# Kernel tuning notes

Measured on AMD Instinct MI355X. Metric: run time of the kernel, lower is better.

## Reference

```python
import jax, jax.numpy as jnp
import numpy as np

N = 100000
E = 1600000
C_IN = 128
C_HID = 128


def setup_inputs() -> dict:
    key = jax.random.key(0)
    ks = jax.random.split(key, 6)
    x = jax.random.normal(ks[0], (N, C_IN), dtype=jnp.float32)
    edge_index = jax.random.randint(ks[1], (2, E), 0, N, dtype=jnp.int64)
    # GCNConv params: linear weight + bias per layer (glorot-ish scale)
    W1 = jax.random.normal(ks[2], (C_IN, C_HID), dtype=jnp.float32) / np.sqrt(C_IN)
    b1 = jnp.zeros((C_HID,), dtype=jnp.float32)
    W2 = jax.random.normal(ks[3], (C_HID, C_HID), dtype=jnp.float32) / np.sqrt(C_HID)
    b2 = jnp.zeros((C_HID,), dtype=jnp.float32)
    return {"x": x, "edge_index": edge_index, "W1": W1, "b1": b1, "W2": W2, "b2": b2}


def _gcn_conv(x, W, b, src, dst, n_nodes):
    # PyG GCNConv: h = D^{-1/2} (A + I) D^{-1/2} (x W) + b
    h = x @ W  # [N, C_out]
    # add self-loops
    loop = jnp.arange(n_nodes, dtype=src.dtype)
    s = jnp.concatenate([src, loop])
    d = jnp.concatenate([dst, loop])
    ones = jnp.ones(s.shape[0], dtype=h.dtype)
    deg = jax.ops.segment_sum(ones, d, num_segments=n_nodes)  # in-degree incl self-loop
    dinv = jnp.where(deg > 0, jax.lax.rsqrt(deg), 0.0)
    norm = dinv[s] * dinv[d]  # [E+N]
    msg = h[s] * norm[:, None]  # gather + scale
    out = jax.ops.segment_sum(msg, d, num_segments=n_nodes)  # scatter-add
    return out + b


def reference(x, edge_index, W1, b1, W2, b2):
    src, dst = edge_index[0], edge_index[1]
    h = jax.nn.relu(_gcn_conv(x, W1, b1, src, dst, N))
    h = jax.nn.relu(_gcn_conv(h, W2, b2, src, dst, N))
    return h
```

## Files before the change

kernel.cpp:

```cpp
#include <hip/hip_runtime.h>
#include <hip/hip_bf16.h>

#define GCN_N 100000
#define GB1 1563
#define NBUCK 782
#define BCAP 4096
#define KPWG 391

typedef unsigned short u16;
typedef unsigned int u32;
typedef float f32x4 __attribute__((ext_vector_type(4)));
typedef short bf16x8 __attribute__((ext_vector_type(8)));

union v16 { uint4 u; bf16x8 h; };

__device__ inline u16 f2bf(float f) {
    u32 u = __float_as_uint(f);
    return (u16)((u + 0x7fffu + ((u >> 16) & 1u)) >> 16);
}
__device__ inline u32 pack2(float a, float b) {
    return (u32)f2bf(a) | ((u32)f2bf(b) << 16);
}
__device__ inline float bf_lo(u32 u) { return __uint_as_float(u << 16); }
__device__ inline float bf_hi(u32 u) { return __uint_as_float(u & 0xffff0000u); }

__device__ inline void addu8(float* a, float4 v) {
    u32 u;
    u = __float_as_uint(v.x); a[0] += bf_lo(u); a[1] += bf_hi(u);
    u = __float_as_uint(v.y); a[2] += bf_lo(u); a[3] += bf_hi(u);
    u = __float_as_uint(v.z); a[4] += bf_lo(u); a[5] += bf_hi(u);
    u = __float_as_uint(v.w); a[6] += bf_lo(u); a[7] += bf_hi(u);
}
__device__ inline void setu8(float* a, float4 v) {
    u32 u;
    u = __float_as_uint(v.x); a[0] = bf_lo(u); a[1] = bf_hi(u);
    u = __float_as_uint(v.y); a[2] = bf_lo(u); a[3] = bf_hi(u);
    u = __float_as_uint(v.z); a[4] = bf_lo(u); a[5] = bf_hi(u);
    u = __float_as_uint(v.w); a[6] = bf_lo(u); a[7] = bf_hi(u);
}

__device__ inline void mfma16(f32x4& d, uint4 a, uint4 b) {
    v16 av, bv; av.u = a; bv.u = b;
    d = __builtin_amdgcn_mfma_f32_16x16x32_bf16(av.h, bv.h, d, 0, 0, 0);
}

__global__ __launch_bounds__(256) void k_init(int* __restrict__ gcursor,
                                              const float* __restrict__ W1,
                                              const float* __restrict__ W2,
                                              u16* __restrict__ Wt1,
                                              u16* __restrict__ Wt2) {
    if (blockIdx.x == 0) {
        for (int i = threadIdx.x; i < NBUCK; i += 256) gcursor[i] = 0;
        return;
    }
    const float* W = (blockIdx.x == 1) ? W1 : W2;
    u16* Wt = (blockIdx.x == 1) ? Wt1 : Wt2;
    for (int i = threadIdx.x; i < 16384; i += 256) {
        int k = i >> 7, nn = i & 127;
        Wt[nn * 128 + k] = f2bf(W[i]);
    }
}

__global__ __launch_bounds__(256) void k_part(const int* __restrict__ src,
                                              const int* __restrict__ dst,
                                              int* __restrict__ gcursor,
                                              u32* __restrict__ part, int E) {
    __shared__ int lhist[NBUCK];
    __shared__ int lbase[NBUCK];
    __shared__ int lcur[NBUCK];
    const int t = threadIdx.x;
    for (int i = t; i < NBUCK; i += 256) { lhist[i] = 0; lcur[i] = 0; }
    __syncthreads();
    const long long e0 = (long long)blockIdx.x * 4096;
    #pragma unroll
    for (int i = 0; i < 16; ++i) {
        long long e = e0 + i * 256 + t;
        if (e < E) atomicAdd(&lhist[dst[e] >> 7], 1);
    }
    __syncthreads();
    for (int i = t; i < NBUCK; i += 256) {
        int c = lhist[i];
        lbase[i] = c ? atomicAdd(&gcursor[i], c) : 0;
    }
    __syncthreads();
    #pragma unroll
    for (int i = 0; i < 16; ++i) {
        long long e = e0 + i * 256 + t;
        if (e < E) {
            int d = dst[e];
            int b = d >> 7;
            int ofs = lbase[b] + atomicAdd(&lcur[b], 1);
            if (ofs < BCAP)
                part[(long long)b * BCAP + ofs] =
                    (u32)src[e] | ((u32)(d & 127) << 17);
        }
    }
}

__global__ __launch_bounds__(256) void k_csr(const int* __restrict__ gcursor,
                                             const u32* __restrict__ part,
                                             int* __restrict__ rowstart,
                                             float* __restrict__ dinv,
                                             int* __restrict__ csr, int n) {
    __shared__ int lcount[128];
    __shared__ int lpfx[128];
    __shared__ int lcur[128];
    __shared__ int wpart[4];
    __shared__ int sbase;
    const int t = threadIdx.x;
    const int lane = t & 63, wid = t >> 6;
    const int b = blockIdx.x;
    int ps = 0;
    for (int j = t; j < b; j += 256) ps += min(gcursor[j], BCAP);
    #pragma unroll
    for (int off = 32; off > 0; off >>= 1) ps += __shfl_down(ps, off, 64);
    if (lane == 0) wpart[wid] = ps;
    if (t < 128) { lcount[t] = 0; lcur[t] = 0; }
    __syncthreads();
    if (t == 0) sbase = wpart[0] + wpart[1] + wpart[2] + wpart[3];
    __syncthreads();
    const int base = sbase;
    const int cnt = min(gcursor[b], BCAP);
    const u32* bp = part + (long long)b * BCAP;
    for (int i = t; i < cnt; i += 256) atomicAdd(&lcount[bp[i] >> 17], 1);
    __syncthreads();
    if (t == 0) {
        int run = 0;
        #pragma unroll
        for (int j = 0; j < 128; ++j) { lpfx[j] = run; run += lcount[j]; }
    }
    __syncthreads();
    int node = b * 128 + t;
    if (t < 128 && node < n) {
        rowstart[node] = base + lpfx[t];
        dinv[node] = rsqrtf((float)(lcount[t] + 1));
    }
    if (b == NBUCK - 1 && t == 0) rowstart[n] = base + cnt;
    for (int i = t; i < cnt; i += 256) {
        u32 v = bp[i];
        int loc = v >> 17;
        int p = base + lpfx[loc] + atomicAdd(&lcur[loc], 1);
        csr[p] = (int)(v & 0x1FFFFu);
    }
}

__device__ __attribute__((always_inline))
inline void gemm_core(const uint4* Xs, const u16* __restrict__ Wt,
                      const float* __restrict__ dinv, u16* __restrict__ H,
                      long long row0, int n) {
    const int t = threadIdx.x;
    const int wid = t >> 6;
    const int l = t & 63, lm = l & 15, lh = l >> 4;
    uint4 a[4];
    const int lrow = wid * 16 + lm;
    #pragma unroll
    for (int kk = 0; kk < 4; ++kk) {
        int byte = (lrow * 256 + kk * 64 + lh * 16) ^ ((lm & 7) << 4);
        a[kk] = Xs[byte >> 4];
    }
    const uint4* wb = (const uint4*)Wt;
    f32x4 acc[8];
    #pragma unroll
    for (int j = 0; j < 8; ++j) acc[j] = (f32x4){0.f, 0.f, 0.f, 0.f};
    #pragma unroll
    for (int j = 0; j < 8; ++j) {
        #pragma unroll
        for (int kk = 0; kk < 4; ++kk) {
            uint4 b = wb[(j * 16 + lm) * 16 + kk * 4 + lh];
            mfma16(acc[j], a[kk], b);
        }
    }
    long long gr0 = row0 + wid * 16 + lh * 4;
    float dv[4];
    #pragma unroll
    for (int r = 0; r < 4; ++r) dv[r] = (gr0 + r < n) ? dinv[gr0 + r] : 0.f;
    #pragma unroll
    for (int j = 0; j < 8; ++j) {
        #pragma unroll
        for (int r = 0; r < 4; ++r) {
            long long grow = gr0 + r;
            if (grow < n) H[grow * 128 + j * 16 + lm] = f2bf(acc[j][r] * dv[r]);
        }
    }
}

__global__ __launch_bounds__(256) void k_gemm1(
        const float* __restrict__ X, const u16* __restrict__ Wt,
        const float* __restrict__ dinv, u16* __restrict__ H, int n) {
    __shared__ uint4 Xs[1024];
    const long long row0 = (long long)blockIdx.x * 64;
    const int t = threadIdx.x;
    uint2* Xs2 = (uint2*)Xs;
    #pragma unroll
    for (int i = 0; i < 8; ++i) {
        int idx = i * 1024 + t * 4;
        int row = idx >> 7, k = idx & 127;
        long long grow = row0 + row; if (grow >= n) grow = n - 1;
        float4 v = *(const float4*)(X + grow * 128 + k);
        int byte = (row * 256 + k * 2) ^ ((row & 7) << 4);
        uint2 p; p.x = pack2(v.x, v.y); p.y = pack2(v.z, v.w);
        Xs2[byte >> 3] = p;
    }
    __syncthreads();
    gemm_core(Xs, Wt, dinv, H, row0, n);
}

__global__ __launch_bounds__(256) void k_gemm2(
        const u16* __restrict__ X, const u16* __restrict__ Wt,
        const float* __restrict__ dinv, u16* __restrict__ H, int n) {
    __shared__ uint4 Xs[1024];
    const long long row0 = (long long)blockIdx.x * 64;
    const int t = threadIdx.x;
    #pragma unroll
    for (int i = 0; i < 4; ++i) {
        int idx = i * 2048 + t * 8;
        int row = idx >> 7, k = idx & 127;
        long long grow = row0 + row; if (grow >= n) grow = n - 1;
        uint4 v = *(const uint4*)(X + grow * 128 + k);
        int byte = (row * 256 + k * 2) ^ ((row & 7) << 4);
        Xs[byte >> 4] = v;
    }
    __syncthreads();
    gemm_core(Xs, Wt, dinv, H, row0, n);
}

template<int OUT_BF16>
__global__ __launch_bounds__(256) void k_agg(const u16* __restrict__ h,
                                             const int* __restrict__ rowstart,
                                             const int* __restrict__ csr_src,
                                             const float* __restrict__ dinv,
                                             const float* __restrict__ bias,
                                             void* __restrict__ outp, int n) {
    const int q    = threadIdx.x >> 4;
    const int sub  = threadIdx.x & 15;
    const int node = blockIdx.x * 16 + q;
    if (node >= n) return;
    const float di = dinv[node];
    int e = rowstart[node];
    const int end = rowstart[node + 1];
    const float4* __restrict__ hv = (const float4*)h;
    float a[8], b[8];
    setu8(a, hv[(size_t)node * 16 + sub]);
    #pragma unroll
    for (int j = 0; j < 8; ++j) b[j] = 0.f;
    for (; e + 8 <= end; e += 8) {
        int s0 = csr_src[e + 0], s1 = csr_src[e + 1];
        int s2 = csr_src[e + 2], s3 = csr_src[e + 3];
        int s4 = csr_src[e + 4], s5 = csr_src[e + 5];
        int s6 = csr_src[e + 6], s7 = csr_src[e + 7];
        float4 v0 = hv[(size_t)s0 * 16 + sub];
        float4 v1 = hv[(size_t)s1 * 16 + sub];
        float4 v2 = hv[(size_t)s2 * 16 + sub];
        float4 v3 = hv[(size_t)s3 * 16 + sub];
        float4 v4 = hv[(size_t)s4 * 16 + sub];
        float4 v5 = hv[(size_t)s5 * 16 + sub];
        float4 v6 = hv[(size_t)s6 * 16 + sub];
        float4 v7 = hv[(size_t)s7 * 16 + sub];
        addu8(a, v0); addu8(b, v1); addu8(a, v2); addu8(b, v3);
        addu8(a, v4); addu8(b, v5); addu8(a, v6); addu8(b, v7);
    }
    for (; e + 4 <= end; e += 4) {
        int s0 = csr_src[e + 0], s1 = csr_src[e + 1];
        int s2 = csr_src[e + 2], s3 = csr_src[e + 3];
        float4 v0 = hv[(size_t)s0 * 16 + sub];
        float4 v1 = hv[(size_t)s1 * 16 + sub];
        float4 v2 = hv[(size_t)s2 * 16 + sub];
        float4 v3 = hv[(size_t)s3 * 16 + sub];
        addu8(a, v0); addu8(b, v1); addu8(a, v2); addu8(b, v3);
    }
    for (; e < end; ++e) {
        float4 v = hv[(size_t)csr_src[e] * 16 + sub];
        addu8(a, v);
    }
    const float4 bv0 = ((const float4*)bias)[sub * 2];
    const float4 bv1 = ((const float4*)bias)[sub * 2 + 1];
    float o[8];
    o[0] = fmaxf(fmaf(a[0] + b[0], di, bv0.x), 0.f);
    o[1] = fmaxf(fmaf(a[1] + b[1], di, bv0.y), 0.f);
    o[2] = fmaxf(fmaf(a[2] + b[2], di, bv0.z), 0.f);
    o[3] = fmaxf(fmaf(a[3] + b[3], di, bv0.w), 0.f);
    o[4] = fmaxf(fmaf(a[4] + b[4], di, bv1.x), 0.f);
    o[5] = fmaxf(fmaf(a[5] + b[5], di, bv1.y), 0.f);
    o[6] = fmaxf(fmaf(a[6] + b[6], di, bv1.z), 0.f);
    o[7] = fmaxf(fmaf(a[7] + b[7], di, bv1.w), 0.f);
    if (OUT_BF16) {
        float4 pv;
        pv.x = __uint_as_float(pack2(o[0], o[1]));
        pv.y = __uint_as_float(pack2(o[2], o[3]));
        pv.z = __uint_as_float(pack2(o[4], o[5]));
        pv.w = __uint_as_float(pack2(o[6], o[7]));
        ((float4*)outp)[(size_t)node * 16 + sub] = pv;
    } else {
        float* out = (float*)outp + (size_t)node * 128 + sub * 8;
        float4 w0 = {o[0], o[1], o[2], o[3]};
        float4 w1 = {o[4], o[5], o[6], o[7]};
        *(float4*)(out + 0) = w0;
        *(float4*)(out + 4) = w1;
    }
}


extern "C" void kernel_launch(void* const* d_in, const int* in_sizes, int n_in,
                              void* d_out, int out_size, void* d_ws, size_t ws_size,
                              hipStream_t stream) {
    const float* x   = (const float*)d_in[0];
    const int* edges = (const int*)d_in[1];
    const float* W1  = (const float*)d_in[2];
    const float* b1  = (const float*)d_in[3];
    const float* W2  = (const float*)d_in[4];
    const float* b2  = (const float*)d_in[5];
    const int E = in_sizes[1] / 2;
    const int N = GCN_N;
    const int* srcp = edges;
    const int* dstp = edges + E;

    char* ws = (char*)d_ws;
    int*   gcursor  = (int*)(ws + 0);
    int*   rowstart = (int*)(ws + 4096);
    float* dinvp    = (float*)(ws + 409600 + 4096);
    u16*   wt1      = (u16*)(ws + 819200);
    u16*   wt2      = (u16*)(ws + 851968);
    u32*   part     = (u32*)(ws + 1048576);
    int*   csr      = (int*)(ws + 14680064);
    u16*   h1       = (u16*)(ws + 23068672);
    u16*   h2       = (u16*)(ws + 50331648);

    k_init<<<3, 256, 0, stream>>>(gcursor, W1, W2, wt1, wt2);
    k_part<<<KPWG, 256, 0, stream>>>(srcp, dstp, gcursor, part, E);
    k_csr<<<NBUCK, 256, 0, stream>>>(gcursor, part, rowstart, dinvp, csr, N);
    k_gemm1<<<GB1, 256, 0, stream>>>(x, wt1, dinvp, h1, N);
    k_agg<1><<<(N + 15) / 16, 256, 0, stream>>>(h1, rowstart, csr, dinvp, b1, h2, N);
    k_gemm2<<<GB1, 256, 0, stream>>>(h2, wt2, dinvp, h1, N);
    k_agg<0><<<(N + 15) / 16, 256, 0, stream>>>(h1, rowstart, csr, dinvp, b2, d_out, N);
}
```

Measured before the change: 270.8 us.

## Fuse edge partition with first GEMM and move source normalization into aggregation

The GEMM no longer pre-scales rows by dinv. That removes the GEMM's dependency on the CSR/degree pass, so the edge-partition blocks and the first GEMM blocks now run in one combined launch with shared LDS reuse. To compensate, the aggregation loads dinv[src] per edge and does FMAs instead of plain adds, and the self term is scaled by di. This removes one kernel launch and lets the partition work overlap with the GEMM, at the cost of an extra per-edge random 4-byte gather and more ALU work in aggregation. The 4-wide tail loop was also removed.

```diff
diff --git a/kernel.cpp b/kernel.cpp
--- a/kernel.cpp
+++ b/kernel.cpp
@@ -24,13 +24,6 @@
 __device__ inline float bf_lo(u32 u) { return __uint_as_float(u << 16); }
 __device__ inline float bf_hi(u32 u) { return __uint_as_float(u & 0xffff0000u); }
 
-__device__ inline void addu8(float* a, float4 v) {
-    u32 u;
-    u = __float_as_uint(v.x); a[0] += bf_lo(u); a[1] += bf_hi(u);
-    u = __float_as_uint(v.y); a[2] += bf_lo(u); a[3] += bf_hi(u);
-    u = __float_as_uint(v.z); a[4] += bf_lo(u); a[5] += bf_hi(u);
-    u = __float_as_uint(v.w); a[6] += bf_lo(u); a[7] += bf_hi(u);
-}
 __device__ inline void setu8(float* a, float4 v) {
     u32 u;
     u = __float_as_uint(v.x); a[0] = bf_lo(u); a[1] = bf_hi(u);
@@ -61,40 +54,96 @@
     }
 }
 
-__global__ __launch_bounds__(256) void k_part(const int* __restrict__ src,
-                                              const int* __restrict__ dst,
-                                              int* __restrict__ gcursor,
-                                              u32* __restrict__ part, int E) {
-    __shared__ int lhist[NBUCK];
-    __shared__ int lbase[NBUCK];
-    __shared__ int lcur[NBUCK];
+__device__ __attribute__((always_inline))
+inline void gemm_core(const uint4* Xs, const u16* __restrict__ Wt,
+                      u16* __restrict__ H, long long row0, int n) {
     const int t = threadIdx.x;
-    for (int i = t; i < NBUCK; i += 256) { lhist[i] = 0; lcur[i] = 0; }
-    __syncthreads();
-    const long long e0 = (long long)blockIdx.x * 4096;
-    #pragma unroll
-    for (int i = 0; i < 16; ++i) {
-        long long e = e0 + i * 256 + t;
-        if (e < E) atomicAdd(&lhist[dst[e] >> 7], 1);
-    }
-    __syncthreads();
-    for (int i = t; i < NBUCK; i += 256) {
-        int c = lhist[i];
-        lbase[i] = c ? atomicAdd(&gcursor[i], c) : 0;
-    }
-    __syncthreads();
-    #pragma unroll
-    for (int i = 0; i < 16; ++i) {
-        long long e = e0 + i * 256 + t;
-        if (e < E) {
-            int d = dst[e];
-            int b = d >> 7;
-            int ofs = lbase[b] + atomicAdd(&lcur[b], 1);
-            if (ofs < BCAP)
-                part[(long long)b * BCAP + ofs] =
-                    (u32)src[e] | ((u32)(d & 127) << 17);
-        }
-    }
+    const int wid = t >> 6;
+    const int l = t & 63, lm = l & 15, lh = l >> 4;
+    uint4 a[4];
+    const int lrow = wid * 16 + lm;
+    #pragma unroll
+    for (int kk = 0; kk < 4; ++kk) {
+        int byte = (lrow * 256 + kk * 64 + lh * 16) ^ ((lm & 7) << 4);
+        a[kk] = Xs[byte >> 4];
+    }
+    const uint4* wb = (const uint4*)Wt;
+    f32x4 acc[8];
+    #pragma unroll
+    for (int j = 0; j < 8; ++j) acc[j] = (f32x4){0.f, 0.f, 0.f, 0.f};
+    #pragma unroll
+    for (int j = 0; j < 8; ++j) {
+        #pragma unroll
+        for (int kk = 0; kk < 4; ++kk) {
+            uint4 b = wb[(j * 16 + lm) * 16 + kk * 4 + lh];
+            mfma16(acc[j], a[kk], b);
+        }
+    }
+    long long gr0 = row0 + wid * 16 + lh * 4;
+    #pragma unroll
+    for (int j = 0; j < 8; ++j) {
+        #pragma unroll
+        for (int r = 0; r < 4; ++r) {
+            long long grow = gr0 + r;
+            if (grow < n) H[grow * 128 + j * 16 + lm] = f2bf(acc[j][r]);
+        }
+    }
+}
+
+__global__ __launch_bounds__(256) void k_part_gemm1(
+        const int* __restrict__ src, const int* __restrict__ dst,
+        int* __restrict__ gcursor, u32* __restrict__ part,
+        const float* __restrict__ X, const u16* __restrict__ Wt,
+        u16* __restrict__ H, int E, int n) {
+    __shared__ uint4 Xs[1024];
+    if (blockIdx.x < KPWG) {
+        int* lhist = (int*)Xs;
+        int* lbase = lhist + NBUCK;
+        int* lcur  = lbase + NBUCK;
+        const int t = threadIdx.x;
+        for (int i = t; i < NBUCK; i += 256) { lhist[i] = 0; lcur[i] = 0; }
+        __syncthreads();
+        const long long e0 = (long long)blockIdx.x * 4096;
+        #pragma unroll
+        for (int i = 0; i < 16; ++i) {
+            long long e = e0 + i * 256 + t;
+            if (e < E) atomicAdd(&lhist[dst[e] >> 7], 1);
+        }
+        __syncthreads();
+        for (int i = t; i < NBUCK; i += 256) {
+            int c = lhist[i];
+            lbase[i] = c ? atomicAdd(&gcursor[i], c) : 0;
+        }
+        __syncthreads();
+        #pragma unroll
+        for (int i = 0; i < 16; ++i) {
+            long long e = e0 + i * 256 + t;
+            if (e < E) {
+                int d = dst[e];
+                int b = d >> 7;
+                int ofs = lbase[b] + atomicAdd(&lcur[b], 1);
+                if (ofs < BCAP)
+                    part[(long long)b * BCAP + ofs] =
+                        (u32)src[e] | ((u32)(d & 127) << 17);
+            }
+        }
+        return;
+    }
+    const long long row0 = (long long)(blockIdx.x - KPWG) * 64;
+    const int t = threadIdx.x;
+    uint2* Xs2 = (uint2*)Xs;
+    #pragma unroll
+    for (int i = 0; i < 8; ++i) {
+        int idx = i * 1024 + t * 4;
+        int row = idx >> 7, k = idx & 127;
+        long long grow = row0 + row; if (grow >= n) grow = n - 1;
+        float4 v = *(const float4*)(X + grow * 128 + k);
+        int byte = (row * 256 + k * 2) ^ ((row & 7) << 4);
+        uint2 p; p.x = pack2(v.x, v.y); p.y = pack2(v.z, v.w);
+        Xs2[byte >> 3] = p;
+    }
+    __syncthreads();
+    gemm_core(Xs, Wt, H, row0, n);
 }
 
 __global__ __launch_bounds__(256) void k_csr(const int* __restrict__ gcursor,
@@ -144,70 +193,9 @@
     }
 }
 
-__device__ __attribute__((always_inline))
-inline void gemm_core(const uint4* Xs, const u16* __restrict__ Wt,
-                      const float* __restrict__ dinv, u16* __restrict__ H,
-                      long long row0, int n) {
-    const int t = threadIdx.x;
-    const int wid = t >> 6;
-    const int l = t & 63, lm = l & 15, lh = l >> 4;
-    uint4 a[4];
-    const int lrow = wid * 16 + lm;
-    #pragma unroll
-    for (int kk = 0; kk < 4; ++kk) {
-        int byte = (lrow * 256 + kk * 64 + lh * 16) ^ ((lm & 7) << 4);
-        a[kk] = Xs[byte >> 4];
-    }
-    const uint4* wb = (const uint4*)Wt;
-    f32x4 acc[8];
-    #pragma unroll
-    for (int j = 0; j < 8; ++j) acc[j] = (f32x4){0.f, 0.f, 0.f, 0.f};
-    #pragma unroll
-    for (int j = 0; j < 8; ++j) {
-        #pragma unroll
-        for (int kk = 0; kk < 4; ++kk) {
-            uint4 b = wb[(j * 16 + lm) * 16 + kk * 4 + lh];
-            mfma16(acc[j], a[kk], b);
-        }
-    }
-    long long gr0 = row0 + wid * 16 + lh * 4;
-    float dv[4];
-    #pragma unroll
-    for (int r = 0; r < 4; ++r) dv[r] = (gr0 + r < n) ? dinv[gr0 + r] : 0.f;
-    #pragma unroll
-    for (int j = 0; j < 8; ++j) {
-        #pragma unroll
-        for (int r = 0; r < 4; ++r) {
-            long long grow = gr0 + r;
-            if (grow < n) H[grow * 128 + j * 16 + lm] = f2bf(acc[j][r] * dv[r]);
-        }
-    }
-}
-
-__global__ __launch_bounds__(256) void k_gemm1(
-        const float* __restrict__ X, const u16* __restrict__ Wt,
-        const float* __restrict__ dinv, u16* __restrict__ H, int n) {
-    __shared__ uint4 Xs[1024];
-    const long long row0 = (long long)blockIdx.x * 64;
-    const int t = threadIdx.x;
-    uint2* Xs2 = (uint2*)Xs;
-    #pragma unroll
-    for (int i = 0; i < 8; ++i) {
-        int idx = i * 1024 + t * 4;
-        int row = idx >> 7, k = idx & 127;
-        long long grow = row0 + row; if (grow >= n) grow = n - 1;
-        float4 v = *(const float4*)(X + grow * 128 + k);
-        int byte = (row * 256 + k * 2) ^ ((row & 7) << 4);
-        uint2 p; p.x = pack2(v.x, v.y); p.y = pack2(v.z, v.w);
-        Xs2[byte >> 3] = p;
-    }
-    __syncthreads();
-    gemm_core(Xs, Wt, dinv, H, row0, n);
-}
-
 __global__ __launch_bounds__(256) void k_gemm2(
         const u16* __restrict__ X, const u16* __restrict__ Wt,
-        const float* __restrict__ dinv, u16* __restrict__ H, int n) {
+        u16* __restrict__ H, int n) {
     __shared__ uint4 Xs[1024];
     const long long row0 = (long long)blockIdx.x * 64;
     const int t = threadIdx.x;
@@ -221,7 +209,7 @@
         Xs[byte >> 4] = v;
     }
     __syncthreads();
-    gemm_core(Xs, Wt, dinv, H, row0, n);
+    gemm_core(Xs, Wt, H, row0, n);
 }
 
 template<int OUT_BF16>
@@ -239,10 +227,10 @@
     int e = rowstart[node];
     const int end = rowstart[node + 1];
     const float4* __restrict__ hv = (const float4*)h;
-    float a[8], b[8];
-    setu8(a, hv[(size_t)node * 16 + sub]);
-    #pragma unroll
-    for (int j = 0; j < 8; ++j) b[j] = 0.f;
+    float a[8], b[8], tmp[8];
+    setu8(tmp, hv[(size_t)node * 16 + sub]);
+    #pragma unroll
+    for (int j = 0; j < 8; ++j) { a[j] = tmp[j] * di; b[j] = 0.f; }
     for (; e + 8 <= end; e += 8) {
         int s0 = csr_src[e + 0], s1 = csr_src[e + 1];
         int s2 = csr_src[e + 2], s3 = csr_src[e + 3];
@@ -256,21 +244,40 @@
         float4 v5 = hv[(size_t)s5 * 16 + sub];
         float4 v6 = hv[(size_t)s6 * 16 + sub];
         float4 v7 = hv[(size_t)s7 * 16 + sub];
-        addu8(a, v0); addu8(b, v1); addu8(a, v2); addu8(b, v3);
-        addu8(a, v4); addu8(b, v5); addu8(a, v6); addu8(b, v7);
-    }
-    for (; e + 4 <= end; e += 4) {
-        int s0 = csr_src[e + 0], s1 = csr_src[e + 1];
-        int s2 = csr_src[e + 2], s3 = csr_src[e + 3];
-        float4 v0 = hv[(size_t)s0 * 16 + sub];
-        float4 v1 = hv[(size_t)s1 * 16 + sub];
-        float4 v2 = hv[(size_t)s2 * 16 + sub];
-        float4 v3 = hv[(size_t)s3 * 16 + sub];
-        addu8(a, v0); addu8(b, v1); addu8(a, v2); addu8(b, v3);
+        float w0 = dinv[s0], w1 = dinv[s1], w2 = dinv[s2], w3 = dinv[s3];
+        float w4 = dinv[s4], w5 = dinv[s5], w6 = dinv[s6], w7 = dinv[s7];
+        setu8(tmp, v0);
+        #pragma unroll
+        for (int j = 0; j < 8; ++j) a[j] = fmaf(tmp[j], w0, a[j]);
+        setu8(tmp, v1);
+        #pragma unroll
+        for (int j = 0; j < 8; ++j) b[j] = fmaf(tmp[j], w1, b[j]);
+        setu8(tmp, v2);
+        #pragma unroll
+        for (int j = 0; j < 8; ++j) a[j] = fmaf(tmp[j], w2, a[j]);
+        setu8(tmp, v3);
+        #pragma unroll
+        for (int j = 0; j < 8; ++j) b[j] = fmaf(tmp[j], w3, b[j]);
+        setu8(tmp, v4);
+        #pragma unroll
+        for (int j = 0; j < 8; ++j) a[j] = fmaf(tmp[j], w4, a[j]);
+        setu8(tmp, v5);
+        #pragma unroll
+        for (int j = 0; j < 8; ++j) b[j] = fmaf(tmp[j], w5, b[j]);
+        setu8(tmp, v6);
+        #pragma unroll
+        for (int j = 0; j < 8; ++j) a[j] = fmaf(tmp[j], w6, a[j]);
+        setu8(tmp, v7);
+        #pragma unroll
+        for (int j = 0; j < 8; ++j) b[j] = fmaf(tmp[j], w7, b[j]);
     }
     for (; e < end; ++e) {
-        float4 v = hv[(size_t)csr_src[e] * 16 + sub];
-        addu8(a, v);
+        int s = csr_src[e];
+        float4 v = hv[(size_t)s * 16 + sub];
+        float w = dinv[s];
+        setu8(tmp, v);
+        #pragma unroll
+        for (int j = 0; j < 8; ++j) a[j] = fmaf(tmp[j], w, a[j]);
     }
     const float4 bv0 = ((const float4*)bias)[sub * 2];
     const float4 bv1 = ((const float4*)bias)[sub * 2 + 1];
@@ -317,7 +324,7 @@
     char* ws = (char*)d_ws;
     int*   gcursor  = (int*)(ws + 0);
     int*   rowstart = (int*)(ws + 4096);
-    float* dinvp    = (float*)(ws + 409600 + 4096);
+    float* dinvp    = (float*)(ws + 413696);
     u16*   wt1      = (u16*)(ws + 819200);
     u16*   wt2      = (u16*)(ws + 851968);
     u32*   part     = (u32*)(ws + 1048576);
@@ -326,10 +333,10 @@
     u16*   h2       = (u16*)(ws + 50331648);
 
     k_init<<<3, 256, 0, stream>>>(gcursor, W1, W2, wt1, wt2);
-    k_part<<<KPWG, 256, 0, stream>>>(srcp, dstp, gcursor, part, E);
+    k_part_gemm1<<<KPWG + GB1, 256, 0, stream>>>(srcp, dstp, gcursor, part,
+                                                 x, wt1, h1, E, N);
     k_csr<<<NBUCK, 256, 0, stream>>>(gcursor, part, rowstart, dinvp, csr, N);
-    k_gemm1<<<GB1, 256, 0, stream>>>(x, wt1, dinvp, h1, N);
     k_agg<1><<<(N + 15) / 16, 256, 0, stream>>>(h1, rowstart, csr, dinvp, b1, h2, N);
-    k_gemm2<<<GB1, 256, 0, stream>>>(h2, wt2, dinvp, h1, N);
+    k_gemm2<<<GB1, 256, 0, stream>>>(h2, wt2, h1, N);
     k_agg<0><<<(N + 15) / 16, 256, 0, stream>>>(h1, rowstart, csr, dinvp, b2, d_out, N);
 }
```

After: 263.6 us. 2.7% less time.

## Fuse edge partitioning with first GEMM and defer dinv scaling to CSR kernel

Applied to the files above, without the earlier changes.

The edge-bucketing kernel and the first feature GEMM now run as one horizontally fused launch, with block ranges split by blockIdx, so the partition work overlaps the GEMM. Because dinv is not yet known when GEMM1 runs, GEMM1 writes unscaled bf16 H, and the CSR kernel rescales its bucket's 128 rows of H by dinv afterwards. This removes a launch and a serialization point but adds an extra read-modify-write pass over H1 and an extra bf16 rounding step.

```diff
diff --git a/kernel.cpp b/kernel.cpp
--- a/kernel.cpp
+++ b/kernel.cpp
@@ -23,6 +23,9 @@
 }
 __device__ inline float bf_lo(u32 u) { return __uint_as_float(u << 16); }
 __device__ inline float bf_hi(u32 u) { return __uint_as_float(u & 0xffff0000u); }
+__device__ inline u32 scale2(u32 p, float d) {
+    return pack2(bf_lo(p) * d, bf_hi(p) * d);
+}
 
 __device__ inline void addu8(float* a, float4 v) {
     u32 u;
@@ -61,89 +64,7 @@
     }
 }
 
-__global__ __launch_bounds__(256) void k_part(const int* __restrict__ src,
-                                              const int* __restrict__ dst,
-                                              int* __restrict__ gcursor,
-                                              u32* __restrict__ part, int E) {
-    __shared__ int lhist[NBUCK];
-    __shared__ int lbase[NBUCK];
-    __shared__ int lcur[NBUCK];
-    const int t = threadIdx.x;
-    for (int i = t; i < NBUCK; i += 256) { lhist[i] = 0; lcur[i] = 0; }
-    __syncthreads();
-    const long long e0 = (long long)blockIdx.x * 4096;
-    #pragma unroll
-    for (int i = 0; i < 16; ++i) {
-        long long e = e0 + i * 256 + t;
-        if (e < E) atomicAdd(&lhist[dst[e] >> 7], 1);
-    }
-    __syncthreads();
-    for (int i = t; i < NBUCK; i += 256) {
-        int c = lhist[i];
-        lbase[i] = c ? atomicAdd(&gcursor[i], c) : 0;
-    }
-    __syncthreads();
-    #pragma unroll
-    for (int i = 0; i < 16; ++i) {
-        long long e = e0 + i * 256 + t;
-        if (e < E) {
-            int d = dst[e];
-            int b = d >> 7;
-            int ofs = lbase[b] + atomicAdd(&lcur[b], 1);
-            if (ofs < BCAP)
-                part[(long long)b * BCAP + ofs] =
-                    (u32)src[e] | ((u32)(d & 127) << 17);
-        }
-    }
-}
-
-__global__ __launch_bounds__(256) void k_csr(const int* __restrict__ gcursor,
-                                             const u32* __restrict__ part,
-                                             int* __restrict__ rowstart,
-                                             float* __restrict__ dinv,
-                                             int* __restrict__ csr, int n) {
-    __shared__ int lcount[128];
-    __shared__ int lpfx[128];
-    __shared__ int lcur[128];
-    __shared__ int wpart[4];
-    __shared__ int sbase;
-    const int t = threadIdx.x;
-    const int lane = t & 63, wid = t >> 6;
-    const int b = blockIdx.x;
-    int ps = 0;
-    for (int j = t; j < b; j += 256) ps += min(gcursor[j], BCAP);
-    #pragma unroll
-    for (int off = 32; off > 0; off >>= 1) ps += __shfl_down(ps, off, 64);
-    if (lane == 0) wpart[wid] = ps;
-    if (t < 128) { lcount[t] = 0; lcur[t] = 0; }
-    __syncthreads();
-    if (t == 0) sbase = wpart[0] + wpart[1] + wpart[2] + wpart[3];
-    __syncthreads();
-    const int base = sbase;
-    const int cnt = min(gcursor[b], BCAP);
-    const u32* bp = part + (long long)b * BCAP;
-    for (int i = t; i < cnt; i += 256) atomicAdd(&lcount[bp[i] >> 17], 1);
-    __syncthreads();
-    if (t == 0) {
-        int run = 0;
-        #pragma unroll
-        for (int j = 0; j < 128; ++j) { lpfx[j] = run; run += lcount[j]; }
-    }
-    __syncthreads();
-    int node = b * 128 + t;
-    if (t < 128 && node < n) {
-        rowstart[node] = base + lpfx[t];
-        dinv[node] = rsqrtf((float)(lcount[t] + 1));
-    }
-    if (b == NBUCK - 1 && t == 0) rowstart[n] = base + cnt;
-    for (int i = t; i < cnt; i += 256) {
-        u32 v = bp[i];
-        int loc = v >> 17;
-        int p = base + lpfx[loc] + atomicAdd(&lcur[loc], 1);
-        csr[p] = (int)(v & 0x1FFFFu);
-    }
-}
-
+template<int SCALE>
 __device__ __attribute__((always_inline))
 inline void gemm_core(const uint4* Xs, const u16* __restrict__ Wt,
                       const float* __restrict__ dinv, u16* __restrict__ H,
@@ -173,22 +94,60 @@
     long long gr0 = row0 + wid * 16 + lh * 4;
     float dv[4];
     #pragma unroll
-    for (int r = 0; r < 4; ++r) dv[r] = (gr0 + r < n) ? dinv[gr0 + r] : 0.f;
+    for (int r = 0; r < 4; ++r)
+        dv[r] = SCALE ? ((gr0 + r < n) ? dinv[gr0 + r] : 0.f) : 1.f;
     #pragma unroll
     for (int j = 0; j < 8; ++j) {
         #pragma unroll
         for (int r = 0; r < 4; ++r) {
             long long grow = gr0 + r;
-            if (grow < n) H[grow * 128 + j * 16 + lm] = f2bf(acc[j][r] * dv[r]);
-        }
-    }
-}
-
-__global__ __launch_bounds__(256) void k_gemm1(
+            if (grow < n)
+                H[grow * 128 + j * 16 + lm] =
+                    f2bf(SCALE ? acc[j][r] * dv[r] : acc[j][r]);
+        }
+    }
+}
+
+__global__ __launch_bounds__(256) void k_part_gemm1(
+        const int* __restrict__ src, const int* __restrict__ dst,
+        int* __restrict__ gcursor, u32* __restrict__ part,
         const float* __restrict__ X, const u16* __restrict__ Wt,
-        const float* __restrict__ dinv, u16* __restrict__ H, int n) {
+        u16* __restrict__ H, int E, int n) {
     __shared__ uint4 Xs[1024];
-    const long long row0 = (long long)blockIdx.x * 64;
+    if (blockIdx.x < KPWG) {
+        int* lhist = (int*)Xs;
+        int* lbase = lhist + NBUCK;
+        int* lcur  = lbase + NBUCK;
+        const int t = threadIdx.x;
+        for (int i = t; i < NBUCK; i += 256) { lhist[i] = 0; lcur[i] = 0; }
+        __syncthreads();
+        const long long e0 = (long long)blockIdx.x * 4096;
+        #pragma unroll
+        for (int i = 0; i < 16; ++i) {
+            long long e = e0 + i * 256 + t;
+            if (e < E) atomicAdd(&lhist[dst[e] >> 7], 1);
+        }
+        __syncthreads();
+        for (int i = t; i < NBUCK; i += 256) {
+            int c = lhist[i];
+            lbase[i] = c ? atomicAdd(&gcursor[i], c) : 0;
+        }
+        __syncthreads();
+        #pragma unroll
+        for (int i = 0; i < 16; ++i) {
+            long long e = e0 + i * 256 + t;
+            if (e < E) {
+                int d = dst[e];
+                int b = d >> 7;
+                int ofs = lbase[b] + atomicAdd(&lcur[b], 1);
+                if (ofs < BCAP)
+                    part[(long long)b * BCAP + ofs] =
+                        (u32)src[e] | ((u32)(d & 127) << 17);
+            }
+        }
+        return;
+    }
+    const long long row0 = (long long)(blockIdx.x - KPWG) * 64;
     const int t = threadIdx.x;
     uint2* Xs2 = (uint2*)Xs;
     #pragma unroll
@@ -202,7 +161,75 @@
         Xs2[byte >> 3] = p;
     }
     __syncthreads();
-    gemm_core(Xs, Wt, dinv, H, row0, n);
+    gemm_core<0>(Xs, Wt, nullptr, H, row0, n);
+}
+
+__global__ __launch_bounds__(256) void k_csr(const int* __restrict__ gcursor,
+                                             const u32* __restrict__ part,
+                                             int* __restrict__ rowstart,
+                                             float* __restrict__ dinv,
+                                             int* __restrict__ csr,
+                                             u16* __restrict__ h1, int n) {
+    __shared__ int lcount[128];
+    __shared__ int lpfx[128];
+    __shared__ int lcur[128];
+    __shared__ float ldinv[128];
+    __shared__ int wpart[4];
+    __shared__ int sbase;
+    const int t = threadIdx.x;
+    const int lane = t & 63, wid = t >> 6;
+    const int b = blockIdx.x;
+    int ps = 0;
+    for (int j = t; j < b; j += 256) ps += min(gcursor[j], BCAP);
+    #pragma unroll
+    for (int off = 32; off > 0; off >>= 1) ps += __shfl_down(ps, off, 64);
+    if (lane == 0) wpart[wid] = ps;
+    if (t < 128) { lcount[t] = 0; lcur[t] = 0; }
+    __syncthreads();
+    if (t == 0) sbase = wpart[0] + wpart[1] + wpart[2] + wpart[3];
+    __syncthreads();
+    const int base = sbase;
+    const int cnt = min(gcursor[b], BCAP);
+    const u32* bp = part + (long long)b * BCAP;
+    for (int i = t; i < cnt; i += 256) atomicAdd(&lcount[bp[i] >> 17], 1);
+    __syncthreads();
+    if (t == 0) {
+        int run = 0;
+        #pragma unroll
+        for (int j = 0; j < 128; ++j) { lpfx[j] = run; run += lcount[j]; }
+    }
+    __syncthreads();
+    int node = b * 128 + t;
+    if (t < 128) {
+        float dv = rsqrtf((float)(lcount[t] + 1));
+        ldinv[t] = dv;
+        if (node < n) {
+            rowstart[node] = base + lpfx[t];
+            dinv[node] = dv;
+        }
+    }
+    if (b == NBUCK - 1 && t == 0) rowstart[n] = base + cnt;
+    __syncthreads();
+    for (int i = t; i < cnt; i += 256) {
+        u32 v = bp[i];
+        int loc = v >> 17;
+        int p = base + lpfx[loc] + atomicAdd(&lcur[loc], 1);
+        csr[p] = (int)(v & 0x1FFFFu);
+    }
+    uint4* h4 = (uint4*)h1;
+    const long long rbase = (long long)b * 128;
+    for (int i = t; i < 2048; i += 256) {
+        int loc = i >> 4;
+        long long nd = rbase + loc;
+        if (nd < n) {
+            float d = ldinv[loc];
+            long long gi = nd * 16 + (i & 15);
+            uint4 v = h4[gi];
+            v.x = scale2(v.x, d); v.y = scale2(v.y, d);
+            v.z = scale2(v.z, d); v.w = scale2(v.w, d);
+            h4[gi] = v;
+        }
+    }
 }
 
 __global__ __launch_bounds__(256) void k_gemm2(
@@ -221,7 +248,7 @@
         Xs[byte >> 4] = v;
     }
     __syncthreads();
-    gemm_core(Xs, Wt, dinv, H, row0, n);
+    gemm_core<1>(Xs, Wt, dinv, H, row0, n);
 }
 
 template<int OUT_BF16>
@@ -317,7 +344,7 @@
     char* ws = (char*)d_ws;
     int*   gcursor  = (int*)(ws + 0);
     int*   rowstart = (int*)(ws + 4096);
-    float* dinvp    = (float*)(ws + 409600 + 4096);
+    float* dinvp    = (float*)(ws + 413696);
     u16*   wt1      = (u16*)(ws + 819200);
     u16*   wt2      = (u16*)(ws + 851968);
     u32*   part     = (u32*)(ws + 1048576);
@@ -326,9 +353,9 @@
     u16*   h2       = (u16*)(ws + 50331648);
 
     k_init<<<3, 256, 0, stream>>>(gcursor, W1, W2, wt1, wt2);
-    k_part<<<KPWG, 256, 0, stream>>>(srcp, dstp, gcursor, part, E);
-    k_csr<<<NBUCK, 256, 0, stream>>>(gcursor, part, rowstart, dinvp, csr, N);
-    k_gemm1<<<GB1, 256, 0, stream>>>(x, wt1, dinvp, h1, N);
+    k_part_gemm1<<<KPWG + GB1, 256, 0, stream>>>(srcp, dstp, gcursor, part,
+                                                 x, wt1, h1, E, N);
+    k_csr<<<NBUCK, 256, 0, stream>>>(gcursor, part, rowstart, dinvp, csr, h1, N);
     k_agg<1><<<(N + 15) / 16, 256, 0, stream>>>(h1, rowstart, csr, dinvp, b1, h2, N);
     k_gemm2<<<GB1, 256, 0, stream>>>(h2, wt2, dinvp, h1, N);
     k_agg<0><<<(N + 15) / 16, 256, 0, stream>>>(h1, rowstart, csr, dinvp, b2, d_out, N);
```

Result: faster. 259.3 us, median of 2 (-4.2%).
